# Performance work log

Hardware: AMD Instinct MI355X
Metric: run time of the kernel (lower is better)

Reference implementation:

```python
import jax, jax.numpy as jnp
import numpy as np

DIM = 512
HEADS = 8
DIM_HEAD = 64
BLOCKS = 6
EXCHANGES = 3
EPS = 1.1920929e-07  # torch.finfo(float32).eps used by RMSNorm(eps=None)


def _rmsnorm(x, w):
    return x * jax.lax.rsqrt(jnp.mean(x * x, axis=-1, keepdims=True) + EPS) * w


def _attention(x, ctx, nw, wq, wkv, wo):
    # x: [B, i, d] queries; ctx: [B, j, d] context (NOT normalized, as in original)
    B = x.shape[0]
    xn = _rmsnorm(x, nw)
    q = jnp.einsum('bid,ed->bie', xn, wq)
    kv = jnp.einsum('bjd,ed->bje', ctx, wkv)
    k, v = jnp.split(kv, 2, axis=-1)
    heads = lambda t: t.reshape(B, t.shape[1], HEADS, DIM_HEAD).transpose(0, 2, 1, 3)
    q, k, v = heads(q), heads(k), heads(v)
    sim = jnp.einsum('bhid,bhjd->bhij', q, k)  # NOTE: original never applies self.scale
    attn = jax.nn.softmax(sim, axis=-1)
    out = jnp.einsum('bhij,bhjd->bhid', attn, v)
    out = out.transpose(0, 2, 1, 3).reshape(B, -1, HEADS * DIM_HEAD)
    return jnp.einsum('bie,de->bid', out, wo)


def _feedforward(x, nw, kw, kb, vw, vb):
    q = _rmsnorm(x, nw)
    h = jnp.einsum('...d,ed->...e', q, kw) + kb
    sim, gates = jnp.split(h, 2, axis=-1)
    h = sim * jax.nn.gelu(gates, approximate=False)  # F.gelu default = exact erf
    return jnp.einsum('...e,de->...d', h, vw) + vb


def _forward(tokens, attn_norm_w, attn_wq, attn_wkv, attn_wo,
             ff_norm_w, ff_keys_w, ff_keys_b, ff_values_w, ff_values_b,
             res_norm_w, res_wq, res_wkv, res_wo):
    b, n, d = tokens.shape
    tokens = jnp.broadcast_to(tokens[None], (BLOCKS, b, n, d))
    messages = [tokens]
    for _ in range(EXCHANGES):
        flat = tokens.reshape(BLOCKS * b, n, d)
        attended = _attention(flat, flat, attn_norm_w, attn_wq, attn_wkv, attn_wo)
        attended = attended.reshape(BLOCKS, b, n, d)
        retrieved = _feedforward(tokens, ff_norm_w, ff_keys_w, ff_keys_b, ff_values_w, ff_values_b)
        messages += [attended, retrieved]
        packed = jnp.concatenate(messages, axis=0)           # [M, b, n, d]
        M = packed.shape[0]
        # einops: repeat 'm b n d -> (b blocks) n m d'
        ctx = jnp.broadcast_to(packed.transpose(1, 2, 0, 3)[:, None], (b, BLOCKS, n, M, d))
        ctx = ctx.reshape(b * BLOCKS * n, M, d)
        # queries packed '(blocks b) n d' then '* n d' -> [blocks*b*n, 1, d]
        q = tokens.reshape(BLOCKS * b * n, 1, d)
        pooled = _attention(q, ctx, res_norm_w, res_wq, res_wkv, res_wo)
        tokens = pooled.reshape(BLOCKS, b, n, d)
    return tokens


def setup_inputs() -> dict:
    key = jax.random.key(0)
    ks = jax.random.split(key, 12)
    b, n, d = 2, 256, DIM
    di = HEADS * DIM_HEAD
    dff = int(d * 4.0 * 2 / 3)
    s = lambda k, shp, fan: (jax.random.normal(k, shp, jnp.float32) / np.sqrt(fan)).astype(jnp.float32)
    return {
        'tokens': jax.random.normal(ks[0], (b, n, d), jnp.float32),
        'attn_norm_w': 1.0 + 0.05 * jax.random.normal(ks[1], (d,), jnp.float32),
        'attn_wq': s(ks[2], (di, d), d),
        'attn_wkv': s(ks[3], (2 * di, d), d),
        'attn_wo': s(ks[4], (d, di), di),
        'ff_norm_w': 1.0 + 0.05 * jax.random.normal(ks[5], (d,), jnp.float32),
        'ff_keys_w': s(ks[6], (2 * dff, d), d),
        'ff_keys_b': 0.01 * jax.random.normal(ks[7], (2 * dff,), jnp.float32),
        'ff_values_w': s(ks[8], (d, dff), dff),
        'ff_values_b': 0.01 * jax.random.normal(ks[9], (d,), jnp.float32),
        'res_norm_w': 1.0 + 0.05 * jax.random.normal(ks[10], (d,), jnp.float32),
        'res_wq': s(ks[11], (di, d), d),
        'res_wkv': s(jax.random.fold_in(key, 100), (2 * di, d), d),
        'res_wo': s(jax.random.fold_in(key, 101), (d, di), di),
    }


def reference(tokens, attn_norm_w, attn_wq, attn_wkv, attn_wo,
              ff_norm_w, ff_keys_w, ff_keys_b, ff_values_w, ff_values_b,
              res_norm_w, res_wq, res_wkv, res_wo):
    return _forward(tokens, attn_norm_w, attn_wq, attn_wkv, attn_wo,
                    ff_norm_w, ff_keys_w, ff_keys_b, ff_values_w, ff_values_b,
                    res_norm_w, res_wq, res_wkv, res_wo)
```

## Files before the change

kernel.cpp:

```cpp
#include <hip/hip_runtime.h>
#include <math.h>

#define Dm   512
#define Nn_  256
#define Bv   2
#define NTD  1024
#define NH   8
#define DH   64
#define DFF  1365
#define DFF2 2730
#define KFF  1408
#define NFF  2816
#define NMD  14
#define EPSR 1.1920929e-07f

typedef _Float16 h16;
typedef h16  v8h  __attribute__((ext_vector_type(8)));
typedef float v4f __attribute__((ext_vector_type(4)));

__device__ inline h16 f2h(float v) { return (h16)v; }

__device__ inline void glds16(const void* g, void* l) {
    __builtin_amdgcn_global_load_lds((const __attribute__((address_space(1))) void*)g,
                                     (__attribute__((address_space(3))) void*)l, 16, 0, 0);
}

struct GDesc {
    const h16* A;
    const h16* W;
    const float* bias;
    const float* rss;
    float* C;
    h16* Cbf;
    long Apl, Wpl, bfpl;
    int lda, ldw, ldc, Nd, mbase, K, mode, nbx;
};

template <int BM, int BN>
__global__ __launch_bounds__(256) void mega_gemm(GDesc d0, GDesc d1, GDesc d2, GDesc d3,
                                                 int n0, int n01, int n012)
{
    constexpr int NWN = (BN == 128) ? 2 : 1;
    constexpr int NWM = 4 / NWN;
    constexpr int MI = BM / (16 * NWM);
    constexpr int ABUF = BM * 32;
    constexpr int WBUFh = BN * 32;
    constexpr int BUF = 2 * ABUF + 2 * WBUFh;
    constexpr int ASEG = BM / 16;
    constexpr int WSEG = BN / 16;
    constexpr int NSEG = 2 * ASEG + 2 * WSEG;
    __shared__ h16 lds[2 * BUF];

    GDesc d; int lb = blockIdx.x;
    if (lb < n0) d = d0;
    else if (lb < n01) { d = d1; lb -= n0; }
    else if (lb < n012) { d = d2; lb -= n01; }
    else { d = d3; lb -= n012; }
    const int bx = lb % d.nbx;
    const int by = lb / d.nbx;

    const int tid = threadIdx.x;
    const int wid = tid >> 6;
    const int lane = tid & 63;
    const int wm = wid / NWN, wn = wid % NWN;
    const int row16 = lane & 15, quad = lane >> 4;
    const long i0 = (long)bx * BM;
    const long j0 = (long)by * BN;
    const int l4 = lane >> 2;
    const int l2s = ((lane & 3) ^ (l4 & 3)) * 8;
    const int ksw = (quad ^ (row16 & 3)) * 8;

    auto stage = [&](int k0, h16* buf) {
        #pragma unroll
        for (int s = 0; s < NSEG / 4; ++s) {
            const int sg = wid * (NSEG / 4) + s;
            const h16* src;
            int dst;
            if (sg < ASEG) {
                src = d.A + (i0 + sg * 16 + l4) * (long)d.lda + k0 + l2s;
                dst = sg * 512;
            } else if (sg < 2 * ASEG) {
                const int r = sg - ASEG;
                src = d.A + d.Apl + (i0 + r * 16 + l4) * (long)d.lda + k0 + l2s;
                dst = ABUF + r * 512;
            } else if (sg < 2 * ASEG + WSEG) {
                const int r = sg - 2 * ASEG;
                src = d.W + (j0 + r * 16 + l4) * (long)d.ldw + k0 + l2s;
                dst = 2 * ABUF + r * 512;
            } else {
                const int r = sg - 2 * ASEG - WSEG;
                src = d.W + d.Wpl + (j0 + r * 16 + l4) * (long)d.ldw + k0 + l2s;
                dst = 2 * ABUF + WBUFh + r * 512;
            }
            glds16(src, &buf[dst]);
        }
    };

    v4f acc[MI][4];
    #pragma unroll
    for (int a = 0; a < MI; ++a)
        #pragma unroll
        for (int b = 0; b < 4; ++b) acc[a][b] = (v4f){0.f, 0.f, 0.f, 0.f};

    stage(0, lds);
    int cur = 0;
    for (int k0 = 0; k0 < d.K; k0 += 32) {
        __syncthreads();
        h16* cbuf = &lds[cur * BUF];
        if (k0 + 32 < d.K) stage(k0 + 32, &lds[(cur ^ 1) * BUF]);

        v8h af[MI], al[MI];
        #pragma unroll
        for (int mi = 0; mi < MI; ++mi) {
            const int aoff = (wm * (16 * MI) + mi * 16 + row16) * 32 + ksw;
            af[mi] = *(const v8h*)&cbuf[aoff];
            al[mi] = *(const v8h*)&cbuf[ABUF + aoff];
        }
        #pragma unroll
        for (int nj = 0; nj < 4; ++nj) {
            const int boff = (wn * 64 + nj * 16 + row16) * 32 + ksw;
            v8h bh = *(const v8h*)&cbuf[2 * ABUF + boff];
            v8h bl = *(const v8h*)&cbuf[2 * ABUF + WBUFh + boff];
            #pragma unroll
            for (int mi = 0; mi < MI; ++mi) {
                acc[mi][nj] = __builtin_amdgcn_mfma_f32_16x16x32_f16(af[mi], bh, acc[mi][nj], 0, 0, 0);
                acc[mi][nj] = __builtin_amdgcn_mfma_f32_16x16x32_f16(af[mi], bl, acc[mi][nj], 0, 0, 0);
                acc[mi][nj] = __builtin_amdgcn_mfma_f32_16x16x32_f16(al[mi], bh, acc[mi][nj], 0, 0, 0);
            }
        }
        cur ^= 1;
    }

    #pragma unroll
    for (int nj = 0; nj < 4; ++nj) {
        const int col = (int)j0 + wn * 64 + nj * 16 + row16;
        if (col < d.Nd) {
            const float bv = d.bias ? d.bias[col] : 0.f;
            #pragma unroll
            for (int mi = 0; mi < MI; ++mi) {
                #pragma unroll
                for (int r = 0; r < 4; ++r) {
                    const long row = i0 + wm * (16 * MI) + mi * 16 + quad * 4 + r;
                    float v = acc[mi][nj][r];
                    if (d.rss) v *= d.rss[(int)row];
                    v += bv;
                    if (d.mode == 0) {
                        d.C[row * (long)d.ldc + col] = v;
                    } else if (d.mode == 1) {
                        const long idx = row * (long)d.ldc + col;
                        const h16 hi = f2h(v);
                        d.Cbf[idx] = hi; d.Cbf[idx + d.bfpl] = f2h(v - (float)hi);
                    } else if (d.mode == 2) {
                        const long idx = row * (long)d.ldc + col;
                        d.C[idx] = v;
                        const h16 hi = f2h(v);
                        d.Cbf[idx] = hi; d.Cbf[idx + d.bfpl] = f2h(v - (float)hi);
                    } else if (d.mode == 3) {
                        const int rr = (int)row & 1023;
                        const int md = d.mbase * 2 + (rr >> 9);
                        const long orow = (long)(((rr >> 8) & 1) * 256 + (rr & 255)) * NMD + md;
                        d.C[orow * 1024 + col] = v;
                    } else if (d.mode == 4) {
                        const h16 hi = f2h(v);
                        const h16 lo = f2h(v - (float)hi);
                        if (col < 512) {
                            const long idx = row * 512 + col;
                            d.Cbf[idx] = hi; d.Cbf[idx + d.bfpl] = lo;
                        } else {
                            const int c = col - 512;
                            const int bh_ = ((int)(row >> 8)) * 8 + (c >> 6);
                            const long idx = (((long)bh_ * 64 + (c & 63)) << 8) + (row & 255);
                            h16* vtp = (h16*)d.C;
                            vtp[idx] = hi; vtp[idx + d.bfpl] = lo;
                        }
                    } else if (d.mode == 5) {
                        const int g = (int)(row >> 9), bb = ((int)row >> 8) & 1, nn = (int)row & 255;
                        #pragma unroll
                        for (int rep = 0; rep < 3; ++rep) {
                            const long orow = (long)(((g * 3 + rep) * 2 + bb) * 256 + nn);
                            d.C[orow * (long)d.ldc + col] = v;
                        }
                    } else {
                        const float gt = __shfl_xor(v, 1, 64);
                        if ((col & 1) == 0) {
                            const float ge = 0.5f * gt * (1.f + erff(gt * 0.70710678118654752440f));
                            const float out = v * ge;
                            const long idx = row * (long)d.ldc + (col >> 1);
                            const h16 hi = f2h(out);
                            d.Cbf[idx] = hi; d.Cbf[idx + d.bfpl] = f2h(out - (float)hi);
                        }
                    }
                }
            }
        }
    }
}

struct SetupP {
    const float *attn_wq, *attn_wkv, *ff_keys_w, *ff_keys_b, *res_wq, *res_wkv,
                *res_wo, *attn_wo, *ff_values_w, *ff_values_b,
                *attn_norm_w, *ff_norm_w, *res_norm_w, *tok_in;
    h16 *wqb, *wkvb, *fkb, *rqb, *rkvb, *rob, *woTb, *fvwTb, *tokbf;
    float *biasWf, *biasFK, *tokens;
};

__device__ inline void cvt_dev(int idx, const float* x, int Ms, int Ks, int Kp,
                               h16* y, long plane, const float* cs)
{
    const int row = idx / Kp;
    const int col = idx - row * Kp;
    float v = (row < Ms && col < Ks) ? x[(long)row * Ks + col] : 0.f;
    if (cs) v *= cs[col];
    const h16 hi = f2h(v);
    y[idx] = hi;
    y[idx + plane] = f2h(v - (float)hi);
}

__device__ inline void cvtT_dev(int idx, const float* x, int R, int C,
                                h16* y, long plane)
{
    const int row = idx / R;
    const int col = idx - row * R;
    const float v = (row < C) ? x[(long)col * C + row] : 0.f;
    const h16 hi = f2h(v);
    y[idx] = hi;
    y[idx + plane] = f2h(v - (float)hi);
}

__global__ __launch_bounds__(256) void setup_all(SetupP p)
{
    long b = blockIdx.x;
    const int t = threadIdx.x;
    if (b < 1024) { cvt_dev((int)(b * 256 + t), p.attn_wq, 512, 512, 512, p.wqb, 512L * 512, p.attn_norm_w); return; }
    b -= 1024;
    if (b < 2048) { cvt_dev((int)(b * 256 + t), p.attn_wkv, 1024, 512, 512, p.wkvb, 1024L * 512, nullptr); return; }
    b -= 2048;
    if (b < 5504) {
        const int idx = (int)(b * 256 + t);
        const int rr = idx >> 9, col = idx & 511;
        const int i = rr >> 1;
        const int src = (rr & 1) ? i + DFF : i;
        float v = 0.f;
        if (i < DFF) v = p.ff_keys_w[(long)src * 512 + col] * p.ff_norm_w[col];
        const h16 hi = f2h(v);
        p.fkb[idx] = hi;
        p.fkb[idx + (long)NFF * 512] = f2h(v - (float)hi);
        return;
    }
    b -= 5504;
    if (b < 1024) { cvt_dev((int)(b * 256 + t), p.res_wq, 512, 512, 512, p.rqb, 512L * 512, p.res_norm_w); return; }
    b -= 1024;
    if (b < 2048) { cvt_dev((int)(b * 256 + t), p.res_wkv, 1024, 512, 512, p.rkvb, 1024L * 512, nullptr); return; }
    b -= 2048;
    if (b < 1024) { cvt_dev((int)(b * 256 + t), p.res_wo, 512, 512, 512, p.rob, 512L * 512, nullptr); return; }
    b -= 1024;
    if (b < 1024) { cvtT_dev((int)(b * 256 + t), p.attn_wo, 512, 512, p.woTb, 512L * 512); return; }
    b -= 1024;
    if (b < 2816) { cvtT_dev((int)(b * 256 + t), p.ff_values_w, 512, DFF, p.fvwTb, (long)KFF * 512); return; }
    b -= 2816;
    if (b < 4) {
        const int n = (int)(b * 256 + t);
        if (n < 1024) {
            float s = 0.f;
            const float* row = p.res_wkv + (long)n * 512;
            for (int dd = 0; dd < 512; ++dd) s = fmaf(row[dd], p.ff_values_b[dd], s);
            p.biasWf[n] = s;
        }
        return;
    }
    b -= 4;
    if (b < 11) {
        const int rr = (int)(b * 256 + t);
        if (rr < 2752) {
            const int i = rr >> 1;
            const int src = (rr & 1) ? i + DFF : i;
            p.biasFK[rr] = (i < DFF) ? p.ff_keys_b[src] : 0.f;
        }
        return;
    }
    b -= 11;
    {
        const int idx = (int)(b * 256 + t);
        const float v = p.tok_in[idx & (Bv * Nn_ * Dm - 1)];
        p.tokens[idx] = v;
        const h16 hi = f2h(v);
        p.tokbf[idx] = hi;
        p.tokbf[idx + (long)NTD * Dm] = f2h(v - (float)hi);
    }
}
#define SETUP_BLOCKS 18575

__global__ __launch_bounds__(256) void rs_kernel(const float* __restrict__ x,
                                                 float* __restrict__ rs)
{
    const int r = blockIdx.x * 4 + (threadIdx.x >> 6);
    const int lane = threadIdx.x & 63;
    const float* row = x + (long)r * Dm + lane * 8;
    float ss = 0.f;
    #pragma unroll
    for (int i = 0; i < 8; i += 4) {
        const float4 v = *(const float4*)(row + i);
        ss += v.x * v.x + v.y * v.y + v.z * v.z + v.w * v.w;
    }
    #pragma unroll
    for (int off = 32; off > 0; off >>= 1) ss += __shfl_xor(ss, off, 64);
    if (lane == 0) rs[r] = rsqrtf(ss * (1.f / 512.f) + EPSR);
}

__global__ __launch_bounds__(256) void attn_self_mfma(
    const h16* __restrict__ qhl, const h16* __restrict__ khl,
    const h16* __restrict__ vtb, long pl, h16* __restrict__ outbf)
{
    __shared__ h16 kh[4096], kl[4096], vh[4096], vl[4096];
    __shared__ h16 pH[4 * 1024], pL[4 * 1024];

    const int bat = blockIdx.x >> 5;
    const int head = (blockIdx.x >> 2) & 7;
    const int qc = blockIdx.x & 3;
    const int t = threadIdx.x;
    const int w = t >> 6, lane = t & 63;
    const int row16 = lane & 15, quad = lane >> 4;

    v8h qh[2], ql[2];
    {
        const long qrow = (long)bat * 256 + qc * 64 + w * 16 + row16;
        const h16* qp = qhl + qrow * 512 + head * 64 + quad * 8;
        qh[0] = *(const v8h*)qp;        qh[1] = *(const v8h*)(qp + 32);
        ql[0] = *(const v8h*)(qp + pl); ql[1] = *(const v8h*)(qp + pl + 32);
    }

    v4f O[4];
    #pragma unroll
    for (int i = 0; i < 4; ++i) O[i] = (v4f){0.f, 0.f, 0.f, 0.f};
    float m[4] = {-1e30f, -1e30f, -1e30f, -1e30f};
    float l[4] = {0.f, 0.f, 0.f, 0.f};

    const int sj = t >> 3;
    const int sc = t & 7;
    const long kbase = ((long)bat * 256) * 512 + head * 64;
    const long vbase = ((long)(bat * 8 + head) * 64) << 8;

    for (int jc = 0; jc < 256; jc += 64) {
        __syncthreads();
        #pragma unroll
        for (int rep = 0; rep < 2; ++rep) {
            const int row = sj + rep * 32;
            const int dsw = row * 64 + ((sc ^ (row & 7)) * 8);
            const h16* ks = khl + kbase + (long)(jc + row) * 512 + sc * 8;
            const h16* vs = vtb + vbase + ((long)row << 8) + jc + sc * 8;
            *(v8h*)&kh[dsw] = *(const v8h*)ks;
            *(v8h*)&kl[dsw] = *(const v8h*)(ks + pl);
            *(v8h*)&vh[dsw] = *(const v8h*)vs;
            *(v8h*)&vl[dsw] = *(const v8h*)(vs + pl);
        }
        __syncthreads();

        v4f S[4];
        #pragma unroll
        for (int i = 0; i < 4; ++i) S[i] = (v4f){0.f, 0.f, 0.f, 0.f};
        #pragma unroll
        for (int kk = 0; kk < 2; ++kk) {
            #pragma unroll
            for (int tile = 0; tile < 4; ++tile) {
                const int off = (tile * 16 + row16) * 64 + (((kk * 4 + quad) ^ (row16 & 7)) * 8);
                v8h bh = *(const v8h*)&kh[off];
                v8h bl = *(const v8h*)&kl[off];
                S[tile] = __builtin_amdgcn_mfma_f32_16x16x32_f16(qh[kk], bh, S[tile], 0, 0, 0);
                S[tile] = __builtin_amdgcn_mfma_f32_16x16x32_f16(qh[kk], bl, S[tile], 0, 0, 0);
                S[tile] = __builtin_amdgcn_mfma_f32_16x16x32_f16(ql[kk], bh, S[tile], 0, 0, 0);
            }
        }

        float mc[4], sums[4], alpha[4];
        #pragma unroll
        for (int r = 0; r < 4; ++r) {
            float v = fmaxf(fmaxf(S[0][r], S[1][r]), fmaxf(S[2][r], S[3][r]));
            v = fmaxf(v, __shfl_xor(v, 1, 64));
            v = fmaxf(v, __shfl_xor(v, 2, 64));
            v = fmaxf(v, __shfl_xor(v, 4, 64));
            v = fmaxf(v, __shfl_xor(v, 8, 64));
            mc[r] = v;
        }
        #pragma unroll
        for (int r = 0; r < 4; ++r) {
            const float mn = fmaxf(m[r], mc[r]);
            alpha[r] = __expf(m[r] - mn);
            m[r] = mn;
            sums[r] = 0.f;
        }
        #pragma unroll
        for (int tile = 0; tile < 4; ++tile) {
            #pragma unroll
            for (int r = 0; r < 4; ++r) {
                const float p = __expf(S[tile][r] - m[r]);
                S[tile][r] = p;
                sums[r] += p;
            }
        }
        #pragma unroll
        for (int r = 0; r < 4; ++r) {
            float v = sums[r];
            v += __shfl_xor(v, 1, 64);
            v += __shfl_xor(v, 2, 64);
            v += __shfl_xor(v, 4, 64);
            v += __shfl_xor(v, 8, 64);
            l[r] = l[r] * alpha[r] + v;
        }
        #pragma unroll
        for (int tile = 0; tile < 4; ++tile)
            #pragma unroll
            for (int r = 0; r < 4; ++r) O[tile][r] *= alpha[r];

        #pragma unroll
        for (int tile = 0; tile < 4; ++tile) {
            const int chunkcol = tile * 2 + (row16 >> 3);
            #pragma unroll
            for (int r = 0; r < 4; ++r) {
                const int prow = quad * 4 + r;
                const int addr = w * 1024 + prow * 64 +
                                 ((chunkcol ^ (prow & 7)) * 8) + (row16 & 7);
                const float p = S[tile][r];
                const h16 hi = f2h(p);
                pH[addr] = hi;
                pL[addr] = f2h(p - (float)hi);
            }
        }

        #pragma unroll
        for (int kk = 0; kk < 2; ++kk) {
            const int poff = w * 1024 + row16 * 64 + (((kk * 4 + quad) ^ (row16 & 7)) * 8);
            v8h pa = *(const v8h*)&pH[poff];
            v8h pb = *(const v8h*)&pL[poff];
            #pragma unroll
            for (int tile = 0; tile < 4; ++tile) {
                const int off = (tile * 16 + row16) * 64 + (((kk * 4 + quad) ^ (row16 & 7)) * 8);
                v8h vbh = *(const v8h*)&vh[off];
                v8h vbl = *(const v8h*)&vl[off];
                O[tile] = __builtin_amdgcn_mfma_f32_16x16x32_f16(pa, vbh, O[tile], 0, 0, 0);
                O[tile] = __builtin_amdgcn_mfma_f32_16x16x32_f16(pa, vbl, O[tile], 0, 0, 0);
                O[tile] = __builtin_amdgcn_mfma_f32_16x16x32_f16(pb, vbh, O[tile], 0, 0, 0);
            }
        }
    }

    #pragma unroll
    for (int tile = 0; tile < 4; ++tile) {
        const int dim = tile * 16 + row16;
        #pragma unroll
        for (int r = 0; r < 4; ++r) {
            const long grow = (long)bat * 256 + qc * 64 + w * 16 + quad * 4 + r;
            const float v = O[tile][r] / l[r];
            const long idx = grow * 512 + head * 64 + dim;
            const h16 hi = f2h(v);
            outbf[idx] = hi;
            outbf[idx + pl] = f2h(v - (float)hi);
        }
    }
}

template <int M>
__global__ __launch_bounds__(128) void attn_pool_kernel(
    const float* __restrict__ qb, const float* __restrict__ kvc3,
    h16* __restrict__ outbf, long plane)
{
    const int rb = blockIdx.x >> 3;
    const int h = blockIdx.x & 7;
    __shared__ float k_lds[M * 66];
    __shared__ float v_lds[M * 66];
    __shared__ float q_lds[2 * 64];
    __shared__ float p_lds[2 * 64];
    const int t = threadIdx.x;
    const int g = rb >> 8, nn = rb & 255;

    for (int idx = t; idx < M * 64; idx += 128) {
        const int m = idx >> 6, d = idx & 63;
        const long base = ((long)rb * NMD + m) * 1024 + h * DH + d;
        k_lds[m * 66 + d] = kvc3[base];
        v_lds[m * 66 + d] = kvc3[base + 512];
    }
    {
        const int w = t >> 6, dd = t & 63;
        const long iq = (long)(g * 2 + w) * 256 + nn;
        q_lds[t] = qb[iq * Dm + h * DH + dd];
    }
    __syncthreads();

    const int w = t >> 6;
    const int lane = t & 63;
    float s = -1e30f;
    if (lane < M) {
        s = 0.f;
        const float* kr = &k_lds[lane * 66];
        const float* qr = &q_lds[w * 64];
        #pragma unroll
        for (int dd = 0; dd < 64; dd += 2) {
            s = fmaf(qr[dd], kr[dd], s);
            s = fmaf(qr[dd + 1], kr[dd + 1], s);
        }
    }
    float mx = s;
    #pragma unroll
    for (int off = 32; off > 0; off >>= 1) mx = fmaxf(mx, __shfl_xor(mx, off, 64));
    const float p = __expf(s - mx);
    float l = p;
    #pragma unroll
    for (int off = 32; off > 0; off >>= 1) l += __shfl_xor(l, off, 64);
    p_lds[w * 64 + lane] = p / l;

    float o = 0.f;
    const float* pr = &p_lds[w * 64];
    #pragma unroll
    for (int m = 0; m < M; ++m)
        o = fmaf(pr[m], v_lds[m * 66 + lane], o);

    const long iq = (long)(g * 2 + w) * 256 + nn;
    const long oidx = iq * Dm + h * DH + lane;
    const h16 hi = f2h(o);
    outbf[oidx] = hi;
    outbf[oidx + plane] = f2h(o - (float)hi);
}

extern "C" void kernel_launch(void* const* d_in, const int* in_sizes, int n_in,
                              void* d_out, int out_size, void* d_ws, size_t ws_size,
                              hipStream_t stream)
{
    const float* tok_in       = (const float*)d_in[0];
    const float* attn_norm_w  = (const float*)d_in[1];
    const float* attn_wq      = (const float*)d_in[2];
    const float* attn_wkv     = (const float*)d_in[3];
    const float* attn_wo      = (const float*)d_in[4];
    const float* ff_norm_w    = (const float*)d_in[5];
    const float* ff_keys_w    = (const float*)d_in[6];
    const float* ff_keys_b    = (const float*)d_in[7];
    const float* ff_values_w  = (const float*)d_in[8];
    const float* ff_values_b  = (const float*)d_in[9];
    const float* res_norm_w   = (const float*)d_in[10];
    const float* res_wq       = (const float*)d_in[11];
    const float* res_wkv      = (const float*)d_in[12];
    const float* res_wo       = (const float*)d_in[13];

    float* ws = (float*)d_ws;
    float* kvc3   = ws;
    float* tokens = kvc3 + 512L * NMD * 1024;
    float* qbuf   = tokens + (long)NTD * Dm;
    float* biasWf = qbuf + (long)NTD * Dm;
    float* biasFK = biasWf + 1024;
    float* rsbuf  = biasFK + 2752;

    h16* us = (h16*)(rsbuf + 1024);
    const long apl = (long)NTD * Dm;
    const long hpl = (long)NTD * KFF;
    const long w1 = 512L * 512, w2 = 1024L * 512, w3 = (long)NFF * 512;
    const long w5 = (long)KFF * 512;
    const long wa_pl = 1024L * 512;
    const long wf_pl = 1024L * KFF;
    h16* tokbf = us; us += 2 * apl;
    h16* abf   = us; us += 2 * apl;
    h16* hbf   = us; us += 2 * hpl;
    h16* qhl   = us; us += 2 * apl;
    h16* khl   = us; us += 2 * apl;
    h16* vtb   = us; us += 2 * apl;
    h16* wqb   = us; us += 2 * w1;
    h16* wkvb  = us; us += 2 * w2;
    h16* fkb   = us; us += 2 * w3;
    h16* rqb   = us; us += 2 * w1;
    h16* rkvb  = us; us += 2 * w2;
    h16* rob   = us; us += 2 * w1;
    h16* woTb  = us; us += 2 * w1;
    h16* fvwTb = us; us += 2 * w5;
    h16* Wab   = us; us += 2 * wa_pl;
    h16* Wfb   = us; us += 2 * wf_pl;

    {
        SetupP p;
        p.attn_wq = attn_wq; p.attn_wkv = attn_wkv; p.ff_keys_w = ff_keys_w;
        p.ff_keys_b = ff_keys_b; p.res_wq = res_wq; p.res_wkv = res_wkv;
        p.res_wo = res_wo; p.attn_wo = attn_wo; p.ff_values_w = ff_values_w;
        p.ff_values_b = ff_values_b;
        p.attn_norm_w = attn_norm_w; p.ff_norm_w = ff_norm_w; p.res_norm_w = res_norm_w;
        p.tok_in = tok_in;
        p.wqb = wqb; p.wkvb = wkvb; p.fkb = fkb; p.rqb = rqb; p.rkvb = rkvb;
        p.rob = rob; p.woTb = woTb; p.fvwTb = fvwTb; p.tokbf = tokbf;
        p.biasWf = biasWf; p.biasFK = biasFK; p.tokens = tokens;
        setup_all<<<SETUP_BLOCKS, 256, 0, stream>>>(p);
    }

    auto mk = [](const h16* A, long Apl, int lda,
                 const h16* W, long Wpl, int ldw,
                 const float* bias, const float* rss,
                 float* C, int ldc, int Nd,
                 h16* Cbf, long bfpl, int mbase, int K,
                 int mode, int nbx) -> GDesc {
        GDesc d;
        d.A = A; d.Apl = Apl; d.lda = lda;
        d.W = W; d.Wpl = Wpl; d.ldw = ldw;
        d.bias = bias; d.rss = rss; d.C = C; d.ldc = ldc; d.Nd = Nd;
        d.Cbf = Cbf; d.bfpl = bfpl; d.mbase = mbase; d.K = K;
        d.mode = mode; d.nbx = nbx;
        return d;
    };

    {
        GDesc dWf = mk(rkvb, w2, 512, fvwTb, w5, 512, nullptr, nullptr, nullptr, KFF, KFF,
                       Wfb, wf_pl, 0, 512, 1, 16);
        GDesc dWa = mk(rkvb, w2, 512, woTb, w1, 512, nullptr, nullptr, nullptr, 512, 512,
                       Wab, wa_pl, 0, 512, 1, 16);
        GDesc dtokKV = mk(tokbf, apl, 512, rkvb, w2, 512, nullptr, nullptr, kvc3, 1024, 1024,
                          nullptr, 0, 0, 512, 3, 16);
        mega_gemm<64, 64><<<736, 256, 0, stream>>>(dWf, dWa, dtokKV, dtokKV, 352, 480, 736);
    }

    for (int e = 0; e < 3; ++e) {
        rs_kernel<<<256, 256, 0, stream>>>(tokens, rsbuf);
        {
            GDesc dffk = mk(tokbf, apl, 512, fkb,  w3, 512, biasFK, rsbuf, nullptr, KFF, DFF2,
                            hbf, hpl, 0, 512, 6, 16);
            GDesc dwkv = mk(tokbf, apl, 512, wkvb, w2, 512, nullptr, nullptr, (float*)vtb, 1024, 1024,
                            khl, apl, 0, 512, 4, 16);
            GDesc dwq  = mk(tokbf, apl, 512, wqb,  w1, 512, nullptr, rsbuf, nullptr, 512, 512,
                            qhl, apl, 0, 512, 1, 16);
            GDesc drq  = mk(tokbf, apl, 512, rqb,  w1, 512, nullptr, rsbuf, qbuf, 512, 512,
                            nullptr, 0, 0, 512, 0, 16);
            mega_gemm<64, 64><<<1200, 256, 0, stream>>>(dffk, dwkv, dwq, drq, 688, 944, 1072);
        }
        attn_self_mfma<<<128, 256, 0, stream>>>(qhl, khl, vtb, apl, abf);
        {
            GDesc dffvKV = mk(hbf, hpl, KFF, Wfb, wf_pl, KFF, biasWf, nullptr, kvc3, 1024, 1024,
                              nullptr, 0, 2 + 2 * e, KFF, 3, 16);
            GDesc dwoKV  = mk(abf, apl, 512, Wab, wa_pl, 512, nullptr, nullptr, kvc3, 1024, 1024,
                              nullptr, 0, 1 + 2 * e, 512, 3, 16);
            mega_gemm<64, 64><<<512, 256, 0, stream>>>(dffvKV, dwoKV, dwoKV, dwoKV, 256, 512, 512);
        }
        if (e == 0)      attn_pool_kernel<6><<<512 * NH, 128, 0, stream>>>(qbuf, kvc3, abf, apl);
        else if (e == 1) attn_pool_kernel<10><<<512 * NH, 128, 0, stream>>>(qbuf, kvc3, abf, apl);
        else             attn_pool_kernel<14><<<512 * NH, 128, 0, stream>>>(qbuf, kvc3, abf, apl);
        {
            if (e < 2) {
                GDesc dro = mk(abf, apl, 512, rob, w1, 512, nullptr, nullptr, tokens, 512, 512,
                               tokbf, apl, 0, 512, 2, 32);
                mega_gemm<32, 128><<<128, 256, 0, stream>>>(dro, dro, dro, dro, 128, 128, 128);
            } else {
                GDesc dro = mk(abf, apl, 512, rob, w1, 512, nullptr, nullptr, (float*)d_out, 512, 512,
                               nullptr, 0, 0, 512, 5, 32);
                mega_gemm<32, 128><<<128, 256, 0, stream>>>(dro, dro, dro, dro, 128, 128, 128);
            }
        }
    }
}
```

Before: 474.9 us.

## Fuse row sum-of-squares into GEMM epilogue and co-schedule attention with FF-value GEMM

Drops the separate rs_kernel. The output projection GEMM epilogue now accumulates per-row sums of squares with atomics into per-exchange buffers, and the setup kernel seeds the first one. It also removes the fp32 tokens copy. Self-attention and the FF-value GEMM are merged into a single launch whose blocks branch between the two bodies, so the small attention grid overlaps GEMM work. The cost is atomic contention, a shared-memory size fixed by the larger of the two bodies, and a split of the wo GEMM into its own launch.

```diff
diff --git a/kernel.cpp b/kernel.cpp
--- a/kernel.cpp
+++ b/kernel.cpp
@@ -30,6 +30,7 @@
     const h16* W;
     const float* bias;
     const float* rss;
+    float* ssqn;
     float* C;
     h16* Cbf;
     long Apl, Wpl, bfpl;
@@ -37,8 +38,7 @@
 };
 
 template <int BM, int BN>
-__global__ __launch_bounds__(256) void mega_gemm(GDesc d0, GDesc d1, GDesc d2, GDesc d3,
-                                                 int n0, int n01, int n012)
+__device__ void gemm_body(const GDesc& d, int lb, h16* lds)
 {
     constexpr int NWN = (BN == 128) ? 2 : 1;
     constexpr int NWM = 4 / NWN;
@@ -49,13 +49,7 @@
     constexpr int ASEG = BM / 16;
     constexpr int WSEG = BN / 16;
     constexpr int NSEG = 2 * ASEG + 2 * WSEG;
-    __shared__ h16 lds[2 * BUF];
-
-    GDesc d; int lb = blockIdx.x;
-    if (lb < n0) d = d0;
-    else if (lb < n01) { d = d1; lb -= n0; }
-    else if (lb < n012) { d = d2; lb -= n01; }
-    else { d = d3; lb -= n012; }
+
     const int bx = lb % d.nbx;
     const int by = lb / d.nbx;
 
@@ -131,6 +125,12 @@
         cur ^= 1;
     }
 
+    float sqacc[MI][4];
+    #pragma unroll
+    for (int a = 0; a < MI; ++a)
+        #pragma unroll
+        for (int r = 0; r < 4; ++r) sqacc[a][r] = 0.f;
+
     #pragma unroll
     for (int nj = 0; nj < 4; ++nj) {
         const int col = (int)j0 + wn * 64 + nj * 16 + row16;
@@ -142,17 +142,13 @@
                 for (int r = 0; r < 4; ++r) {
                     const long row = i0 + wm * (16 * MI) + mi * 16 + quad * 4 + r;
                     float v = acc[mi][nj][r];
-                    if (d.rss) v *= d.rss[(int)row];
+                    if (d.rss) v *= rsqrtf(d.rss[(int)row] * (1.f / 512.f) + EPSR);
                     v += bv;
+                    if (d.ssqn) sqacc[mi][r] += v * v;
                     if (d.mode == 0) {
                         d.C[row * (long)d.ldc + col] = v;
                     } else if (d.mode == 1) {
                         const long idx = row * (long)d.ldc + col;
-                        const h16 hi = f2h(v);
-                        d.Cbf[idx] = hi; d.Cbf[idx + d.bfpl] = f2h(v - (float)hi);
-                    } else if (d.mode == 2) {
-                        const long idx = row * (long)d.ldc + col;
-                        d.C[idx] = v;
                         const h16 hi = f2h(v);
                         d.Cbf[idx] = hi; d.Cbf[idx + d.bfpl] = f2h(v - (float)hi);
                     } else if (d.mode == 3) {
@@ -194,6 +190,200 @@
             }
         }
     }
+
+    if (d.ssqn) {
+        #pragma unroll
+        for (int mi = 0; mi < MI; ++mi)
+            #pragma unroll
+            for (int r = 0; r < 4; ++r) {
+                float s = sqacc[mi][r];
+                s += __shfl_xor(s, 1, 64);
+                s += __shfl_xor(s, 2, 64);
+                s += __shfl_xor(s, 4, 64);
+                s += __shfl_xor(s, 8, 64);
+                if (row16 == 0) {
+                    const long row = i0 + wm * (16 * MI) + mi * 16 + quad * 4 + r;
+                    atomicAdd(&d.ssqn[row], s);
+                }
+            }
+    }
+}
+
+template <int BM, int BN>
+__global__ __launch_bounds__(256) void mega_gemm(GDesc d0, GDesc d1, GDesc d2, GDesc d3,
+                                                 int n0, int n01, int n012)
+{
+    constexpr int BUF2 = 2 * (2 * BM * 32 + 2 * BN * 32);
+    __shared__ h16 lds[BUF2];
+    GDesc d; int lb = blockIdx.x;
+    if (lb < n0) d = d0;
+    else if (lb < n01) { d = d1; lb -= n0; }
+    else if (lb < n012) { d = d2; lb -= n01; }
+    else { d = d3; lb -= n012; }
+    gemm_body<BM, BN>(d, lb, lds);
+}
+
+__device__ void attn_body(const h16* __restrict__ qhl, const h16* __restrict__ khl,
+                          const h16* __restrict__ vtb, long pl,
+                          h16* __restrict__ outbf, h16* smem)
+{
+    h16* kh = smem;
+    h16* kl = smem + 4096;
+    h16* vh = smem + 8192;
+    h16* vl = smem + 12288;
+    h16* pH = smem + 16384;
+    h16* pL = smem + 20480;
+
+    const int bat = blockIdx.x >> 5;
+    const int head = (blockIdx.x >> 2) & 7;
+    const int qc = blockIdx.x & 3;
+    const int t = threadIdx.x;
+    const int w = t >> 6, lane = t & 63;
+    const int row16 = lane & 15, quad = lane >> 4;
+
+    v8h qh[2], ql[2];
+    {
+        const long qrow = (long)bat * 256 + qc * 64 + w * 16 + row16;
+        const h16* qp = qhl + qrow * 512 + head * 64 + quad * 8;
+        qh[0] = *(const v8h*)qp;        qh[1] = *(const v8h*)(qp + 32);
+        ql[0] = *(const v8h*)(qp + pl); ql[1] = *(const v8h*)(qp + pl + 32);
+    }
+
+    v4f O[4];
+    #pragma unroll
+    for (int i = 0; i < 4; ++i) O[i] = (v4f){0.f, 0.f, 0.f, 0.f};
+    float m[4] = {-1e30f, -1e30f, -1e30f, -1e30f};
+    float l[4] = {0.f, 0.f, 0.f, 0.f};
+
+    const int sj = t >> 3;
+    const int sc = t & 7;
+    const long kbase = ((long)bat * 256) * 512 + head * 64;
+    const long vbase = ((long)(bat * 8 + head) * 64) << 8;
+
+    for (int jc = 0; jc < 256; jc += 64) {
+        __syncthreads();
+        #pragma unroll
+        for (int rep = 0; rep < 2; ++rep) {
+            const int row = sj + rep * 32;
+            const int dsw = row * 64 + ((sc ^ (row & 7)) * 8);
+            const h16* ks = khl + kbase + (long)(jc + row) * 512 + sc * 8;
+            const h16* vs = vtb + vbase + ((long)row << 8) + jc + sc * 8;
+            *(v8h*)&kh[dsw] = *(const v8h*)ks;
+            *(v8h*)&kl[dsw] = *(const v8h*)(ks + pl);
+            *(v8h*)&vh[dsw] = *(const v8h*)vs;
+            *(v8h*)&vl[dsw] = *(const v8h*)(vs + pl);
+        }
+        __syncthreads();
+
+        v4f S[4];
+        #pragma unroll
+        for (int i = 0; i < 4; ++i) S[i] = (v4f){0.f, 0.f, 0.f, 0.f};
+        #pragma unroll
+        for (int kk = 0; kk < 2; ++kk) {
+            #pragma unroll
+            for (int tile = 0; tile < 4; ++tile) {
+                const int off = (tile * 16 + row16) * 64 + (((kk * 4 + quad) ^ (row16 & 7)) * 8);
+                v8h bh = *(const v8h*)&kh[off];
+                v8h bl = *(const v8h*)&kl[off];
+                S[tile] = __builtin_amdgcn_mfma_f32_16x16x32_f16(qh[kk], bh, S[tile], 0, 0, 0);
+                S[tile] = __builtin_amdgcn_mfma_f32_16x16x32_f16(qh[kk], bl, S[tile], 0, 0, 0);
+                S[tile] = __builtin_amdgcn_mfma_f32_16x16x32_f16(ql[kk], bh, S[tile], 0, 0, 0);
+            }
+        }
+
+        float mc[4], sums[4], alpha[4];
+        #pragma unroll
+        for (int r = 0; r < 4; ++r) {
+            float v = fmaxf(fmaxf(S[0][r], S[1][r]), fmaxf(S[2][r], S[3][r]));
+            v = fmaxf(v, __shfl_xor(v, 1, 64));
+            v = fmaxf(v, __shfl_xor(v, 2, 64));
+            v = fmaxf(v, __shfl_xor(v, 4, 64));
+            v = fmaxf(v, __shfl_xor(v, 8, 64));
+            mc[r] = v;
+        }
+        #pragma unroll
+        for (int r = 0; r < 4; ++r) {
+            const float mn = fmaxf(m[r], mc[r]);
+            alpha[r] = __expf(m[r] - mn);
+            m[r] = mn;
+            sums[r] = 0.f;
+        }
+        #pragma unroll
+        for (int tile = 0; tile < 4; ++tile) {
+            #pragma unroll
+            for (int r = 0; r < 4; ++r) {
+                const float p = __expf(S[tile][r] - m[r]);
+                S[tile][r] = p;
+                sums[r] += p;
+            }
+        }
+        #pragma unroll
+        for (int r = 0; r < 4; ++r) {
+            float v = sums[r];
+            v += __shfl_xor(v, 1, 64);
+            v += __shfl_xor(v, 2, 64);
+            v += __shfl_xor(v, 4, 64);
+            v += __shfl_xor(v, 8, 64);
+            l[r] = l[r] * alpha[r] + v;
+        }
+        #pragma unroll
+        for (int tile = 0; tile < 4; ++tile)
+            #pragma unroll
+            for (int r = 0; r < 4; ++r) O[tile][r] *= alpha[r];
+
+        #pragma unroll
+        for (int tile = 0; tile < 4; ++tile) {
+            const int chunkcol = tile * 2 + (row16 >> 3);
+            #pragma unroll
+            for (int r = 0; r < 4; ++r) {
+                const int prow = quad * 4 + r;
+                const int addr = w * 1024 + prow * 64 +
+                                 ((chunkcol ^ (prow & 7)) * 8) + (row16 & 7);
+                const float p = S[tile][r];
+                const h16 hi = f2h(p);
+                pH[addr] = hi;
+                pL[addr] = f2h(p - (float)hi);
+            }
+        }
+
+        #pragma unroll
+        for (int kk = 0; kk < 2; ++kk) {
+            const int poff = w * 1024 + row16 * 64 + (((kk * 4 + quad) ^ (row16 & 7)) * 8);
+            v8h pa = *(const v8h*)&pH[poff];
+            v8h pb = *(const v8h*)&pL[poff];
+            #pragma unroll
+            for (int tile = 0; tile < 4; ++tile) {
+                const int off = (tile * 16 + row16) * 64 + (((kk * 4 + quad) ^ (row16 & 7)) * 8);
+                v8h vbh = *(const v8h*)&vh[off];
+                v8h vbl = *(const v8h*)&vl[off];
+                O[tile] = __builtin_amdgcn_mfma_f32_16x16x32_f16(pa, vbh, O[tile], 0, 0, 0);
+                O[tile] = __builtin_amdgcn_mfma_f32_16x16x32_f16(pa, vbl, O[tile], 0, 0, 0);
+                O[tile] = __builtin_amdgcn_mfma_f32_16x16x32_f16(pb, vbh, O[tile], 0, 0, 0);
+            }
+        }
+    }
+
+    #pragma unroll
+    for (int tile = 0; tile < 4; ++tile) {
+        const int dim = tile * 16 + row16;
+        #pragma unroll
+        for (int r = 0; r < 4; ++r) {
+            const long grow = (long)bat * 256 + qc * 64 + w * 16 + quad * 4 + r;
+            const float v = O[tile][r] / l[r];
+            const long idx = grow * 512 + head * 64 + dim;
+            const h16 hi = f2h(v);
+            outbf[idx] = hi;
+            outbf[idx + pl] = f2h(v - (float)hi);
+        }
+    }
+}
+
+__global__ __launch_bounds__(256) void attn_ffv(
+    GDesc d, const h16* qhl, const h16* khl, const h16* vtb, long pl, h16* outbf)
+{
+    __shared__ h16 smem[24576];
+    if (blockIdx.x < 128) attn_body(qhl, khl, vtb, pl, outbf, smem);
+    else gemm_body<64, 64>(d, blockIdx.x - 128, smem);
 }
 
 struct SetupP {
@@ -201,7 +391,7 @@
                 *res_wo, *attn_wo, *ff_values_w, *ff_values_b,
                 *attn_norm_w, *ff_norm_w, *res_norm_w, *tok_in;
     h16 *wqb, *wkvb, *fkb, *rqb, *rkvb, *rob, *woTb, *fvwTb, *tokbf;
-    float *biasWf, *biasFK, *tokens;
+    float *biasWf, *biasFK, *ssq;
 };
 
 __device__ inline void cvt_dev(int idx, const float* x, int Ms, int Ks, int Kp,
@@ -260,12 +450,10 @@
     b -= 2816;
     if (b < 4) {
         const int n = (int)(b * 256 + t);
-        if (n < 1024) {
-            float s = 0.f;
-            const float* row = p.res_wkv + (long)n * 512;
-            for (int dd = 0; dd < 512; ++dd) s = fmaf(row[dd], p.ff_values_b[dd], s);
-            p.biasWf[n] = s;
-        }
+        float s = 0.f;
+        const float* row = p.res_wkv + (long)n * 512;
+        for (int dd = 0; dd < 512; ++dd) s = fmaf(row[dd], p.ff_values_b[dd], s);
+        p.biasWf[n] = s;
         return;
     }
     b -= 4;
@@ -279,184 +467,29 @@
         return;
     }
     b -= 11;
+    if (b < 4) {
+        const int n = (int)(b * 256 + t);
+        const float* row = p.tok_in + (long)(n & 511) * 512;
+        float s = 0.f;
+        for (int dd = 0; dd < 512; ++dd) s = fmaf(row[dd], row[dd], s);
+        p.ssq[n] = s;
+        return;
+    }
+    b -= 4;
+    if (b < 8) {
+        p.ssq[1024 + (int)(b * 256 + t)] = 0.f;
+        return;
+    }
+    b -= 8;
     {
         const int idx = (int)(b * 256 + t);
         const float v = p.tok_in[idx & (Bv * Nn_ * Dm - 1)];
-        p.tokens[idx] = v;
         const h16 hi = f2h(v);
         p.tokbf[idx] = hi;
         p.tokbf[idx + (long)NTD * Dm] = f2h(v - (float)hi);
     }
 }
-#define SETUP_BLOCKS 18575
-
-__global__ __launch_bounds__(256) void rs_kernel(const float* __restrict__ x,
-                                                 float* __restrict__ rs)
-{
-    const int r = blockIdx.x * 4 + (threadIdx.x >> 6);
-    const int lane = threadIdx.x & 63;
-    const float* row = x + (long)r * Dm + lane * 8;
-    float ss = 0.f;
-    #pragma unroll
-    for (int i = 0; i < 8; i += 4) {
-        const float4 v = *(const float4*)(row + i);
-        ss += v.x * v.x + v.y * v.y + v.z * v.z + v.w * v.w;
-    }
-    #pragma unroll
-    for (int off = 32; off > 0; off >>= 1) ss += __shfl_xor(ss, off, 64);
-    if (lane == 0) rs[r] = rsqrtf(ss * (1.f / 512.f) + EPSR);
-}
-
-__global__ __launch_bounds__(256) void attn_self_mfma(
-    const h16* __restrict__ qhl, const h16* __restrict__ khl,
-    const h16* __restrict__ vtb, long pl, h16* __restrict__ outbf)
-{
-    __shared__ h16 kh[4096], kl[4096], vh[4096], vl[4096];
-    __shared__ h16 pH[4 * 1024], pL[4 * 1024];
-
-    const int bat = blockIdx.x >> 5;
-    const int head = (blockIdx.x >> 2) & 7;
-    const int qc = blockIdx.x & 3;
-    const int t = threadIdx.x;
-    const int w = t >> 6, lane = t & 63;
-    const int row16 = lane & 15, quad = lane >> 4;
-
-    v8h qh[2], ql[2];
-    {
-        const long qrow = (long)bat * 256 + qc * 64 + w * 16 + row16;
-        const h16* qp = qhl + qrow * 512 + head * 64 + quad * 8;
-        qh[0] = *(const v8h*)qp;        qh[1] = *(const v8h*)(qp + 32);
-        ql[0] = *(const v8h*)(qp + pl); ql[1] = *(const v8h*)(qp + pl + 32);
-    }
-
-    v4f O[4];
-    #pragma unroll
-    for (int i = 0; i < 4; ++i) O[i] = (v4f){0.f, 0.f, 0.f, 0.f};
-    float m[4] = {-1e30f, -1e30f, -1e30f, -1e30f};
-    float l[4] = {0.f, 0.f, 0.f, 0.f};
-
-    const int sj = t >> 3;
-    const int sc = t & 7;
-    const long kbase = ((long)bat * 256) * 512 + head * 64;
-    const long vbase = ((long)(bat * 8 + head) * 64) << 8;
-
-    for (int jc = 0; jc < 256; jc += 64) {
-        __syncthreads();
-        #pragma unroll
-        for (int rep = 0; rep < 2; ++rep) {
-            const int row = sj + rep * 32;
-            const int dsw = row * 64 + ((sc ^ (row & 7)) * 8);
-            const h16* ks = khl + kbase + (long)(jc + row) * 512 + sc * 8;
-            const h16* vs = vtb + vbase + ((long)row << 8) + jc + sc * 8;
-            *(v8h*)&kh[dsw] = *(const v8h*)ks;
-            *(v8h*)&kl[dsw] = *(const v8h*)(ks + pl);
-            *(v8h*)&vh[dsw] = *(const v8h*)vs;
-            *(v8h*)&vl[dsw] = *(const v8h*)(vs + pl);
-        }
-        __syncthreads();
-
-        v4f S[4];
-        #pragma unroll
-        for (int i = 0; i < 4; ++i) S[i] = (v4f){0.f, 0.f, 0.f, 0.f};
-        #pragma unroll
-        for (int kk = 0; kk < 2; ++kk) {
-            #pragma unroll
-            for (int tile = 0; tile < 4; ++tile) {
-                const int off = (tile * 16 + row16) * 64 + (((kk * 4 + quad) ^ (row16 & 7)) * 8);
-                v8h bh = *(const v8h*)&kh[off];
-                v8h bl = *(const v8h*)&kl[off];
-                S[tile] = __builtin_amdgcn_mfma_f32_16x16x32_f16(qh[kk], bh, S[tile], 0, 0, 0);
-                S[tile] = __builtin_amdgcn_mfma_f32_16x16x32_f16(qh[kk], bl, S[tile], 0, 0, 0);
-                S[tile] = __builtin_amdgcn_mfma_f32_16x16x32_f16(ql[kk], bh, S[tile], 0, 0, 0);
-            }
-        }
-
-        float mc[4], sums[4], alpha[4];
-        #pragma unroll
-        for (int r = 0; r < 4; ++r) {
-            float v = fmaxf(fmaxf(S[0][r], S[1][r]), fmaxf(S[2][r], S[3][r]));
-            v = fmaxf(v, __shfl_xor(v, 1, 64));
-            v = fmaxf(v, __shfl_xor(v, 2, 64));
-            v = fmaxf(v, __shfl_xor(v, 4, 64));
-            v = fmaxf(v, __shfl_xor(v, 8, 64));
-            mc[r] = v;
-        }
-        #pragma unroll
-        for (int r = 0; r < 4; ++r) {
-            const float mn = fmaxf(m[r], mc[r]);
-            alpha[r] = __expf(m[r] - mn);
-            m[r] = mn;
-            sums[r] = 0.f;
-        }
-        #pragma unroll
-        for (int tile = 0; tile < 4; ++tile) {
-            #pragma unroll
-            for (int r = 0; r < 4; ++r) {
-                const float p = __expf(S[tile][r] - m[r]);
-                S[tile][r] = p;
-                sums[r] += p;
-            }
-        }
-        #pragma unroll
-        for (int r = 0; r < 4; ++r) {
-            float v = sums[r];
-            v += __shfl_xor(v, 1, 64);
-            v += __shfl_xor(v, 2, 64);
-            v += __shfl_xor(v, 4, 64);
-            v += __shfl_xor(v, 8, 64);
-            l[r] = l[r] * alpha[r] + v;
-        }
-        #pragma unroll
-        for (int tile = 0; tile < 4; ++tile)
-            #pragma unroll
-            for (int r = 0; r < 4; ++r) O[tile][r] *= alpha[r];
-
-        #pragma unroll
-        for (int tile = 0; tile < 4; ++tile) {
-            const int chunkcol = tile * 2 + (row16 >> 3);
-            #pragma unroll
-            for (int r = 0; r < 4; ++r) {
-                const int prow = quad * 4 + r;
-                const int addr = w * 1024 + prow * 64 +
-                                 ((chunkcol ^ (prow & 7)) * 8) + (row16 & 7);
-                const float p = S[tile][r];
-                const h16 hi = f2h(p);
-                pH[addr] = hi;
-                pL[addr] = f2h(p - (float)hi);
-            }
-        }
-
-        #pragma unroll
-        for (int kk = 0; kk < 2; ++kk) {
-            const int poff = w * 1024 + row16 * 64 + (((kk * 4 + quad) ^ (row16 & 7)) * 8);
-            v8h pa = *(const v8h*)&pH[poff];
-            v8h pb = *(const v8h*)&pL[poff];
-            #pragma unroll
-            for (int tile = 0; tile < 4; ++tile) {
-                const int off = (tile * 16 + row16) * 64 + (((kk * 4 + quad) ^ (row16 & 7)) * 8);
-                v8h vbh = *(const v8h*)&vh[off];
-                v8h vbl = *(const v8h*)&vl[off];
-                O[tile] = __builtin_amdgcn_mfma_f32_16x16x32_f16(pa, vbh, O[tile], 0, 0, 0);
-                O[tile] = __builtin_amdgcn_mfma_f32_16x16x32_f16(pa, vbl, O[tile], 0, 0, 0);
-                O[tile] = __builtin_amdgcn_mfma_f32_16x16x32_f16(pb, vbh, O[tile], 0, 0, 0);
-            }
-        }
-    }
-
-    #pragma unroll
-    for (int tile = 0; tile < 4; ++tile) {
-        const int dim = tile * 16 + row16;
-        #pragma unroll
-        for (int r = 0; r < 4; ++r) {
-            const long grow = (long)bat * 256 + qc * 64 + w * 16 + quad * 4 + r;
-            const float v = O[tile][r] / l[r];
-            const long idx = grow * 512 + head * 64 + dim;
-            const h16 hi = f2h(v);
-            outbf[idx] = hi;
-            outbf[idx + pl] = f2h(v - (float)hi);
-        }
-    }
-}
+#define SETUP_BLOCKS 18587
 
 template <int M>
 __global__ __launch_bounds__(128) void attn_pool_kernel(
@@ -541,13 +574,12 @@
 
     float* ws = (float*)d_ws;
     float* kvc3   = ws;
-    float* tokens = kvc3 + 512L * NMD * 1024;
-    float* qbuf   = tokens + (long)NTD * Dm;
+    float* qbuf   = kvc3 + 512L * NMD * 1024;
     float* biasWf = qbuf + (long)NTD * Dm;
     float* biasFK = biasWf + 1024;
-    float* rsbuf  = biasFK + 2752;
-
-    h16* us = (h16*)(rsbuf + 1024);
+    float* ssq    = biasFK + 2752;
+
+    h16* us = (h16*)(ssq + 3 * 1024);
     const long apl = (long)NTD * Dm;
     const long hpl = (long)NTD * KFF;
     const long w1 = 512L * 512, w2 = 1024L * 512, w3 = (long)NFF * 512;
@@ -581,67 +613,71 @@
         p.tok_in = tok_in;
         p.wqb = wqb; p.wkvb = wkvb; p.fkb = fkb; p.rqb = rqb; p.rkvb = rkvb;
         p.rob = rob; p.woTb = woTb; p.fvwTb = fvwTb; p.tokbf = tokbf;
-        p.biasWf = biasWf; p.biasFK = biasFK; p.tokens = tokens;
+        p.biasWf = biasWf; p.biasFK = biasFK; p.ssq = ssq;
         setup_all<<<SETUP_BLOCKS, 256, 0, stream>>>(p);
     }
 
     auto mk = [](const h16* A, long Apl, int lda,
                  const h16* W, long Wpl, int ldw,
-                 const float* bias, const float* rss,
+                 const float* bias, const float* rss, float* ssqn,
                  float* C, int ldc, int Nd,
                  h16* Cbf, long bfpl, int mbase, int K,
                  int mode, int nbx) -> GDesc {
         GDesc d;
         d.A = A; d.Apl = Apl; d.lda = lda;
         d.W = W; d.Wpl = Wpl; d.ldw = ldw;
-        d.bias = bias; d.rss = rss; d.C = C; d.ldc = ldc; d.Nd = Nd;
+        d.bias = bias; d.rss = rss; d.ssqn = ssqn;
+        d.C = C; d.ldc = ldc; d.Nd = Nd;
         d.Cbf = Cbf; d.bfpl = bfpl; d.mbase = mbase; d.K = K;
         d.mode = mode; d.nbx = nbx;
         return d;
     };
 
     {
-        GDesc dWf = mk(rkvb, w2, 512, fvwTb, w5, 512, nullptr, nullptr, nullptr, KFF, KFF,
-                       Wfb, wf_pl, 0, 512, 1, 16);
-        GDesc dWa = mk(rkvb, w2, 512, woTb, w1, 512, nullptr, nullptr, nullptr, 512, 512,
-                       Wab, wa_pl, 0, 512, 1, 16);
-        GDesc dtokKV = mk(tokbf, apl, 512, rkvb, w2, 512, nullptr, nullptr, kvc3, 1024, 1024,
-                          nullptr, 0, 0, 512, 3, 16);
+        GDesc dWf = mk(rkvb, w2, 512, fvwTb, w5, 512, nullptr, nullptr, nullptr,
+                       nullptr, KFF, KFF, Wfb, wf_pl, 0, 512, 1, 16);
+        GDesc dWa = mk(rkvb, w2, 512, woTb, w1, 512, nullptr, nullptr, nullptr,
+                       nullptr, 512, 512, Wab, wa_pl, 0, 512, 1, 16);
+        GDesc dtokKV = mk(tokbf, apl, 512, rkvb, w2, 512, nullptr, nullptr, nullptr,
+                          kvc3, 1024, 1024, nullptr, 0, 0, 512, 3, 16);
         mega_gemm<64, 64><<<736, 256, 0, stream>>>(dWf, dWa, dtokKV, dtokKV, 352, 480, 736);
     }
 
     for (int e = 0; e < 3; ++e) {
-        rs_kernel<<<256, 256, 0, stream>>>(tokens, rsbuf);
+        float* rse = ssq + (long)e * 1024;
         {
-            GDesc dffk = mk(tokbf, apl, 512, fkb,  w3, 512, biasFK, rsbuf, nullptr, KFF, DFF2,
-                            hbf, hpl, 0, 512, 6, 16);
-            GDesc dwkv = mk(tokbf, apl, 512, wkvb, w2, 512, nullptr, nullptr, (float*)vtb, 1024, 1024,
-                            khl, apl, 0, 512, 4, 16);
-            GDesc dwq  = mk(tokbf, apl, 512, wqb,  w1, 512, nullptr, rsbuf, nullptr, 512, 512,
-                            qhl, apl, 0, 512, 1, 16);
-            GDesc drq  = mk(tokbf, apl, 512, rqb,  w1, 512, nullptr, rsbuf, qbuf, 512, 512,
-                            nullptr, 0, 0, 512, 0, 16);
+            GDesc dffk = mk(tokbf, apl, 512, fkb,  w3, 512, biasFK, rse, nullptr,
+                            nullptr, KFF, DFF2, hbf, hpl, 0, 512, 6, 16);
+            GDesc dwkv = mk(tokbf, apl, 512, wkvb, w2, 512, nullptr, nullptr, nullptr,
+                            (float*)vtb, 1024, 1024, khl, apl, 0, 512, 4, 16);
+            GDesc dwq  = mk(tokbf, apl, 512, wqb,  w1, 512, nullptr, rse, nullptr,
+                            nullptr, 512, 512, qhl, apl, 0, 512, 1, 16);
+            GDesc drq  = mk(tokbf, apl, 512, rqb,  w1, 512, nullptr, rse, nullptr,
+                            qbuf, 512, 512, nullptr, 0, 0, 512, 0, 16);
             mega_gemm<64, 64><<<1200, 256, 0, stream>>>(dffk, dwkv, dwq, drq, 688, 944, 1072);
         }
-        attn_self_mfma<<<128, 256, 0, stream>>>(qhl, khl, vtb, apl, abf);
         {
-            GDesc dffvKV = mk(hbf, hpl, KFF, Wfb, wf_pl, KFF, biasWf, nullptr, kvc3, 1024, 1024,
-                              nullptr, 0, 2 + 2 * e, KFF, 3, 16);
-            GDesc dwoKV  = mk(abf, apl, 512, Wab, wa_pl, 512, nullptr, nullptr, kvc3, 1024, 1024,
-                              nullptr, 0, 1 + 2 * e, 512, 3, 16);
-            mega_gemm<64, 64><<<512, 256, 0, stream>>>(dffvKV, dwoKV, dwoKV, dwoKV, 256, 512, 512);
+            GDesc dffvKV = mk(hbf, hpl, KFF, Wfb, wf_pl, KFF, biasWf, nullptr, nullptr,
+                              kvc3, 1024, 1024, nullptr, 0, 2 + 2 * e, KFF, 3, 16);
+            attn_ffv<<<384, 256, 0, stream>>>(dffvKV, qhl, khl, vtb, apl, abf);
+        }
+        {
+            GDesc dwoKV = mk(abf, apl, 512, Wab, wa_pl, 512, nullptr, nullptr, nullptr,
+                             kvc3, 1024, 1024, nullptr, 0, 1 + 2 * e, 512, 3, 16);
+            mega_gemm<64, 64><<<256, 256, 0, stream>>>(dwoKV, dwoKV, dwoKV, dwoKV, 256, 256, 256);
         }
         if (e == 0)      attn_pool_kernel<6><<<512 * NH, 128, 0, stream>>>(qbuf, kvc3, abf, apl);
         else if (e == 1) attn_pool_kernel<10><<<512 * NH, 128, 0, stream>>>(qbuf, kvc3, abf, apl);
         else             attn_pool_kernel<14><<<512 * NH, 128, 0, stream>>>(qbuf, kvc3, abf, apl);
         {
             if (e < 2) {
-                GDesc dro = mk(abf, apl, 512, rob, w1, 512, nullptr, nullptr, tokens, 512, 512,
-                               tokbf, apl, 0, 512, 2, 32);
+                GDesc dro = mk(abf, apl, 512, rob, w1, 512, nullptr, nullptr,
+                               ssq + (long)(e + 1) * 1024,
+                               nullptr, 512, 512, tokbf, apl, 0, 512, 1, 32);
                 mega_gemm<32, 128><<<128, 256, 0, stream>>>(dro, dro, dro, dro, 128, 128, 128);
             } else {
-                GDesc dro = mk(abf, apl, 512, rob, w1, 512, nullptr, nullptr, (float*)d_out, 512, 512,
-                               nullptr, 0, 0, 512, 5, 32);
+                GDesc dro = mk(abf, apl, 512, rob, w1, 512, nullptr, nullptr, nullptr,
+                               (float*)d_out, 512, 512, nullptr, 0, 0, 512, 5, 32);
                 mega_gemm<32, 128><<<128, 256, 0, stream>>>(dro, dro, dro, dro, 128, 128, 128);
             }
         }
```

Result: faster. 465.5 us (-2.0%).
